# Optimization experiments

Hardware: AMD Instinct MI355X
Metric: run time of the kernel (lower is better)

## Reference

```python
import jax, jax.numpy as jnp
import numpy as np

N = 100000   # nodes
E = 1600000  # edges
FEAT = 128
HID = 128
TGT = 64
L = 3
G = 512      # graphs in batch


def setup_inputs() -> dict:
    key = jax.random.key(0)
    ks = jax.random.split(key, 16)
    s = 0.05
    return {
        "x": jax.random.normal(ks[0], (N, FEAT), jnp.float32),
        "edge_index": jax.random.randint(ks[1], (2, E), 0, N, dtype=jnp.int32),
        "batch": jnp.sort(jax.random.randint(ks[2], (N,), 0, G, dtype=jnp.int32)),
        "conv_w1": jax.random.normal(ks[3], (L, FEAT, HID), jnp.float32) * s,
        "conv_b1": jax.random.normal(ks[4], (L, HID), jnp.float32) * s,
        "conv_w2": jax.random.normal(ks[5], (L, HID, HID), jnp.float32) * s,
        "conv_b2": jax.random.normal(ks[6], (L, HID), jnp.float32) * s,
        "eps": jnp.zeros((L,), jnp.float32),
        "gn_scale": jnp.ones((L, HID), jnp.float32),
        "gn_weight": jnp.ones((L, HID), jnp.float32),
        "gn_bias": jnp.zeros((L, HID), jnp.float32),
        "proj_w1": jax.random.normal(ks[7], (L, HID, HID), jnp.float32) * s,
        "proj_b1": jax.random.normal(ks[8], (L, HID), jnp.float32) * s,
        "proj_w2": jax.random.normal(ks[9], (L, HID, TGT), jnp.float32) * s,
        "proj_b2": jax.random.normal(ks[10], (L, TGT), jnp.float32) * s,
    }


def _graph_norm(h, batch, counts, scale, weight, bias):
    # per-graph mean -> scatter back to nodes
    mean = jax.ops.segment_sum(h, batch, num_segments=G) / counts
    sub = h - mean[batch] * scale
    var = jax.ops.segment_sum(sub * sub, batch, num_segments=G) / counts
    std = jnp.sqrt(var + 1e-8)
    return weight * sub / std[batch] + bias


def reference(x, edge_index, batch, conv_w1, conv_b1, conv_w2, conv_b2, eps,
              gn_scale, gn_weight, gn_bias, proj_w1, proj_b1, proj_w2, proj_b2):
    src, dst = edge_index[0], edge_index[1]
    counts = jnp.maximum(
        jax.ops.segment_sum(jnp.ones((N, 1), x.dtype), batch, num_segments=G), 1.0)
    h = x
    z_cat = []
    for l in range(L):
        # GINConv: aggr_j->i then 2-layer MLP
        aggr = jax.ops.segment_sum(h[src], dst, num_segments=N)
        h = (1.0 + eps[l]) * h + aggr
        h = jax.nn.relu(h @ conv_w1[l] + conv_b1[l]) @ conv_w2[l] + conv_b2[l]
        # GraphNorm
        h = _graph_norm(h, batch, counts, gn_scale[l], gn_weight[l], gn_bias[l])
        h = jax.nn.relu(h)
        # projection MLP + global add pool
        z = jax.nn.relu(h @ proj_w1[l] + proj_b1[l]) @ proj_w2[l] + proj_b2[l]
        z_cat.append(jax.ops.segment_sum(z, batch, num_segments=G))
    return jnp.concatenate(z_cat, axis=-1)  # [G, L*TGT]
```

## Files before the change

### kernel.cpp

```cpp
#include <hip/hip_runtime.h>

#define NN 100000
#define EE 1600000
#define HIDD 128
#define TGTT 64
#define GGG 512
#define NBK 98
#define CAPB 17408
#define ABLK 800
#define EPB 2000
#define CVT2 512
#define LSTR 136
#define GBLK 782
#define OUTB 128

typedef unsigned short ushort_t;
typedef __attribute__((ext_vector_type(8))) short short8;
typedef __attribute__((ext_vector_type(4))) float f32x4;
typedef __attribute__((ext_vector_type(4))) unsigned short us4;

__device__ __forceinline__ float b2f(ushort_t u) {
    union { unsigned int i; float f; } v; v.i = ((unsigned int)u) << 16; return v.f;
}
__device__ __forceinline__ ushort_t f2b(float f) {
    union { float f; unsigned int i; } v; v.f = f;
    unsigned int r = (v.i + 0x7fffu + ((v.i >> 16) & 1u)) >> 16;
    return (ushort_t)r;
}

__global__ __launch_bounds__(256) void k_pro(const float* __restrict__ x, ushort_t* __restrict__ Xb,
                                             const float* __restrict__ cw1, const float* __restrict__ cw2,
                                             const float* __restrict__ pw1, ushort_t* __restrict__ Wt,
                                             const int* __restrict__ batch, int* __restrict__ goff,
                                             const int* __restrict__ ei, int* __restrict__ gcnt,
                                             unsigned int* __restrict__ bbuf) {
    __shared__ int cnt[NBK], base[NBK], cur[NBK];
    int b = blockIdx.x, t = threadIdx.x;

    if (b < ABLK) {
        if (t < NBK) cnt[t] = 0;
        __syncthreads();
        int e0 = b * EPB;
        int e1 = min(e0 + EPB, EE);
        for (int e = e0 + t; e < e1; e += 256)
            atomicAdd(&cnt[ei[EE + e] >> 10], 1);
        __syncthreads();
        if (t < NBK) { base[t] = atomicAdd(&gcnt[t], cnt[t]); cur[t] = 0; }
        __syncthreads();
        for (int e = e0 + t; e < e1; e += 256) {
            int s = ei[e], d = ei[EE + e];
            int bk = d >> 10;
            int off = base[bk] + atomicAdd(&cur[bk], 1);
            if (off < CAPB)
                bbuf[(long)bk * CAPB + off] = (unsigned int)s | (((unsigned int)d & 1023u) << 17);
        }
        return;
    }
    b -= ABLK;
    if (b < CVT2) {
        long total = (long)NN * HIDD / 4;
        long step = (long)CVT2 * 256;
        for (long i = (long)b * 256 + t; i < total; i += step) {
            float4 v = ((const float4*)x)[i];
            us4 o; o.x = f2b(v.x); o.y = f2b(v.y); o.z = f2b(v.z); o.w = f2b(v.w);
            ((us4*)Xb)[i] = o;
        }
        return;
    }
    b -= CVT2;
    if (b < 9) {
        int l = b / 3, j = b % 3;
        const float* src = (j == 0 ? cw1 : j == 1 ? cw2 : pw1) + (size_t)l * HIDD * HIDD;
        ushort_t* dst = Wt + (size_t)b * HIDD * HIDD;
        for (int i = t; i < HIDD * HIDD; i += 256)
            dst[(i & 127) * HIDD + (i >> 7)] = f2b(src[i]);
        return;
    }
    b -= 9;
    {
        int g = b * 256 + t;
        if (g > GGG) return;
        int lo = 0, hi = NN;
        while (lo < hi) { int mid = (lo + hi) >> 1; if (batch[mid] < g) lo = mid + 1; else hi = mid; }
        goff[g] = lo;
    }
}

__global__ __launch_bounds__(1024) void k_csr(const int* __restrict__ gcnt,
                                              const unsigned int* __restrict__ bbuf,
                                              int* __restrict__ rowptr, int* __restrict__ csr) {
    __shared__ int ldeg[1024], tsum[1024], sb[NBK];
    int b = blockIdx.x, t = threadIdx.x;
    if (t < NBK) sb[t] = gcnt[t];
    ldeg[t] = 0;
    __syncthreads();
    if (t == 0) { int a = 0; for (int i = 0; i < NBK; i++) { int v = sb[i]; sb[i] = a; a += v; } }
    __syncthreads();
    int cnt = min(gcnt[b], CAPB);
    int base = sb[b];
    const unsigned int* bb = bbuf + (long)b * CAPB;
    for (int i = t; i < cnt; i += 1024) atomicAdd(&ldeg[bb[i] >> 17], 1);
    __syncthreads();
    int d0 = ldeg[t];
    tsum[t] = d0;
    __syncthreads();
    for (int off = 1; off < 1024; off <<= 1) {
        int u = (t >= off) ? tsum[t - off] : 0;
        __syncthreads();
        tsum[t] += u;
        __syncthreads();
    }
    int p0 = base + tsum[t] - d0;
    int gnode = b * 1024 + t;
    if (gnode < NN) rowptr[gnode] = p0;
    if (b == NBK - 1 && t == 0) rowptr[NN] = EE;
    ldeg[t] = p0;
    __syncthreads();
    for (int i = t; i < cnt; i += 1024) {
        unsigned int en = bb[i];
        int pos = atomicAdd(&ldeg[en >> 17], 1);
        csr[pos] = (int)(en & 0x1FFFFu);
    }
}

__global__ __launch_bounds__(256) void k_gmlp(const ushort_t* __restrict__ hin,
                                              const int* __restrict__ rowptr,
                                              const int* __restrict__ csr,
                                              const float* __restrict__ eps, int l,
                                              const ushort_t* __restrict__ Wt1, const float* __restrict__ B1,
                                              const ushort_t* __restrict__ Wt2, const float* __restrict__ B2,
                                              ushort_t* __restrict__ Y,
                                              const float* __restrict__ pooledP, const int* __restrict__ goff,
                                              const float* __restrict__ WoP, const float* __restrict__ BoP,
                                              float* __restrict__ outP, int lprev) {
    __shared__ ushort_t sX[128 * LSTR];
    int tid = threadIdx.x;

    if (blockIdx.x >= GBLK) {
        if (lprev < 0) return;
        int ob = blockIdx.x - GBLK;
        int sub = tid >> 6, tt = tid & 63;
        int g = ob * 4 + sub;
        if (g >= GGG) return;
        float cntg = (float)(goff[g + 1] - goff[g]);
        float acc = cntg * BoP[tt];
        const float* p = pooledP + (long)g * HIDD;
        for (int k = 0; k < HIDD; k++) acc += p[k] * WoP[k * TGTT + tt];
        outP[(long)g * (3 * TGTT) + lprev * TGTT + tt] = acc;
        return;
    }

    long base = (long)blockIdx.x * 128;
    int lane = tid & 15, ng = tid >> 4;
    int off = lane << 3;
    float e1 = 1.0f + eps[l];

#pragma unroll 1
    for (int it = 0; it < 8; it++) {
        int row = it * 16 + ng;
        long node = base + row;
        short8 o = (short8)0;
        if (node < NN) {
            short8 h = *(const short8*)(hin + (node << 7) + off);
            float acc[8];
#pragma unroll
            for (int t = 0; t < 8; t++) acc[t] = e1 * b2f((ushort_t)h[t]);
            int jb = rowptr[node], je = rowptr[node + 1];
            int j = jb;
            for (; j + 8 <= je; j += 8) {
                int s0 = csr[j], s1 = csr[j + 1], s2 = csr[j + 2], s3 = csr[j + 3];
                int s4 = csr[j + 4], s5 = csr[j + 5], s6 = csr[j + 6], s7 = csr[j + 7];
                short8 v0 = *(const short8*)(hin + ((long)s0 << 7) + off);
                short8 v1 = *(const short8*)(hin + ((long)s1 << 7) + off);
                short8 v2 = *(const short8*)(hin + ((long)s2 << 7) + off);
                short8 v3 = *(const short8*)(hin + ((long)s3 << 7) + off);
                short8 v4 = *(const short8*)(hin + ((long)s4 << 7) + off);
                short8 v5 = *(const short8*)(hin + ((long)s5 << 7) + off);
                short8 v6 = *(const short8*)(hin + ((long)s6 << 7) + off);
                short8 v7 = *(const short8*)(hin + ((long)s7 << 7) + off);
#pragma unroll
                for (int t = 0; t < 8; t++)
                    acc[t] += ((b2f((ushort_t)v0[t]) + b2f((ushort_t)v1[t])) +
                               (b2f((ushort_t)v2[t]) + b2f((ushort_t)v3[t]))) +
                              ((b2f((ushort_t)v4[t]) + b2f((ushort_t)v5[t])) +
                               (b2f((ushort_t)v6[t]) + b2f((ushort_t)v7[t])));
            }
            for (; j + 4 <= je; j += 4) {
                int s0 = csr[j], s1 = csr[j + 1], s2 = csr[j + 2], s3 = csr[j + 3];
                short8 v0 = *(const short8*)(hin + ((long)s0 << 7) + off);
                short8 v1 = *(const short8*)(hin + ((long)s1 << 7) + off);
                short8 v2 = *(const short8*)(hin + ((long)s2 << 7) + off);
                short8 v3 = *(const short8*)(hin + ((long)s3 << 7) + off);
#pragma unroll
                for (int t = 0; t < 8; t++)
                    acc[t] += (b2f((ushort_t)v0[t]) + b2f((ushort_t)v1[t])) +
                              (b2f((ushort_t)v2[t]) + b2f((ushort_t)v3[t]));
            }
            for (; j < je; j++) {
                int s = csr[j];
                short8 v = *(const short8*)(hin + ((long)s << 7) + off);
#pragma unroll
                for (int t = 0; t < 8; t++) acc[t] += b2f((ushort_t)v[t]);
            }
#pragma unroll
            for (int t = 0; t < 8; t++) o[t] = (short)f2b(acc[t]);
        }
        *(short8*)(sX + row * LSTR + off) = o;
    }
    __syncthreads();

    int w = tid >> 6, l64 = tid & 63, q = l64 >> 4, l16 = l64 & 15;
    int r0 = w * 16, r1 = 64 + w * 16;
    short8 a0[4], a1[4];
#pragma unroll
    for (int c = 0; c < 4; c++) {
        a0[c] = *(const short8*)(sX + (r0 + l16) * LSTR + q * 8 + c * 32);
        a1[c] = *(const short8*)(sX + (r1 + l16) * LSTR + q * 8 + c * 32);
    }
    f32x4 acc0[8], acc1[8];
#pragma unroll
    for (int nt = 0; nt < 8; nt++) {
        int col = nt * 16 + l16;
        float bias = B1[col];
        f32x4 c0 = {bias, bias, bias, bias};
        f32x4 c1 = c0;
        const ushort_t* bB = Wt1 + col * HIDD + q * 8;
#pragma unroll
        for (int c = 0; c < 4; c++) {
            short8 b = *(const short8*)(bB + c * 32);
            c0 = __builtin_amdgcn_mfma_f32_16x16x32_bf16(a0[c], b, c0, 0, 0, 0);
            c1 = __builtin_amdgcn_mfma_f32_16x16x32_bf16(a1[c], b, c1, 0, 0, 0);
        }
        acc0[nt] = c0; acc1[nt] = c1;
    }
#pragma unroll
    for (int nt = 0; nt < 8; nt++) {
        int col = nt * 16 + l16;
#pragma unroll
        for (int r = 0; r < 4; r++) {
            sX[(r0 + q * 4 + r) * LSTR + col] = f2b(fmaxf(acc0[nt][r], 0.f));
            sX[(r1 + q * 4 + r) * LSTR + col] = f2b(fmaxf(acc1[nt][r], 0.f));
        }
    }
#pragma unroll
    for (int c = 0; c < 4; c++) {
        a0[c] = *(const short8*)(sX + (r0 + l16) * LSTR + q * 8 + c * 32);
        a1[c] = *(const short8*)(sX + (r1 + l16) * LSTR + q * 8 + c * 32);
    }
#pragma unroll
    for (int nt = 0; nt < 8; nt++) {
        int col = nt * 16 + l16;
        float bias = B2[col];
        f32x4 c0 = {bias, bias, bias, bias};
        f32x4 c1 = c0;
        const ushort_t* bB = Wt2 + col * HIDD + q * 8;
#pragma unroll
        for (int c = 0; c < 4; c++) {
            short8 b = *(const short8*)(bB + c * 32);
            c0 = __builtin_amdgcn_mfma_f32_16x16x32_bf16(a0[c], b, c0, 0, 0, 0);
            c1 = __builtin_amdgcn_mfma_f32_16x16x32_bf16(a1[c], b, c1, 0, 0, 0);
        }
#pragma unroll
        for (int r = 0; r < 4; r++) {
            long row0 = base + r0 + q * 4 + r;
            long row1 = base + r1 + q * 4 + r;
            if (row0 < NN) Y[(row0 << 7) + col] = f2b(c0[r]);
            if (row1 < NN) Y[(row1 << 7) + col] = f2b(c1[r]);
        }
    }
}

__global__ __launch_bounds__(512) void k_gstat(const ushort_t* __restrict__ Hraw,
                                               const int* __restrict__ goff,
                                               const float* __restrict__ scale,
                                               const float* __restrict__ weight,
                                               const float* __restrict__ gnb,
                                               float* __restrict__ Ab, float* __restrict__ Bb,
                                               float* __restrict__ pooled) {
    __shared__ float red[2][32][128];
    int g = blockIdx.x;
    int s = goff[g], e = goff[g + 1];
    float cnt = (float)max(e - s, 1);
    int lane = threadIdx.x & 15;
    int rg = threadIdx.x >> 4;
    int f0 = lane << 3;
    float sum[8], sq[8];
#pragma unroll
    for (int t = 0; t < 8; t++) { sum[t] = 0.f; sq[t] = 0.f; }
    for (int i = s + rg; i < e; i += 32) {
        short8 v = *(const short8*)(Hraw + ((long)i << 7) + f0);
#pragma unroll
        for (int t = 0; t < 8; t++) { float a = b2f((ushort_t)v[t]); sum[t] += a; sq[t] += a * a; }
    }
#pragma unroll
    for (int t = 0; t < 8; t++) { red[0][rg][f0 + t] = sum[t]; red[1][rg][f0 + t] = sq[t]; }
    __syncthreads();
    for (int off = 16; off > 0; off >>= 1) {
        if (rg < off) {
#pragma unroll
            for (int t = 0; t < 8; t++) {
                red[0][rg][f0 + t] += red[0][rg + off][f0 + t];
                red[1][rg][f0 + t] += red[1][rg + off][f0 + t];
            }
        }
        __syncthreads();
    }
    if (rg == 0) {
#pragma unroll
        for (int t = 0; t < 8; t++) {
            int f = f0 + t;
            float mean = red[0][0][f] / cnt;
            float ms = mean * scale[f];
            float var = red[1][0][f] / cnt - 2.f * ms * mean + ms * ms;
            float A = weight[f] / sqrtf(var + 1e-8f);
            Ab[g * HIDD + f] = A;
            Bb[g * HIDD + f] = gnb[f] - ms * A;
            pooled[g * HIDD + f] = 0.f;
        }
    }
}

__global__ __launch_bounds__(256) void k_projpool(const ushort_t* __restrict__ Hraw,
                                                  const int* __restrict__ batch,
                                                  const float* __restrict__ Ab, const float* __restrict__ Bb,
                                                  const ushort_t* __restrict__ Wt, const float* __restrict__ B,
                                                  ushort_t* __restrict__ Hn, float* __restrict__ pooled,
                                                  int store_hn) {
    __shared__ ushort_t sX[128 * LSTR];
    __shared__ int sgid[128];
    __shared__ float sA[4][128], sB[4][128];
    int tid = threadIdx.x;
    long base = (long)blockIdx.x * 128;

    if (tid < 128) sgid[tid] = (base + tid < NN) ? batch[base + tid] : -1;
    __syncthreads();
    int gmin = sgid[0];
    {
        int f = tid & 127;
#pragma unroll
        for (int s = tid >> 7; s < 4; s += 2) {
            int gg = gmin + s;
            if (gg < GGG) {
                sA[s][f] = Ab[(long)gg * HIDD + f];
                sB[s][f] = Bb[(long)gg * HIDD + f];
            }
        }
    }
    __syncthreads();

#pragma unroll
    for (int c = 0; c < 8; c++) {
        int idx = c * 256 + tid;
        int row = idx >> 4, cw = idx & 15;
        long grow = base + row;
        short8 v = (short8)0;
        if (grow < NN) {
            short8 raw = *(const short8*)(Hraw + (grow << 7) + (cw << 3));
            int slot = sgid[row] - gmin;
            const float* pA = &sA[slot][cw << 3];
            const float* pB = &sB[slot][cw << 3];
#pragma unroll
            for (int t = 0; t < 8; t++) {
                float val = b2f((ushort_t)raw[t]) * pA[t] + pB[t];
                v[t] = (short)f2b(val > 0.f ? val : 0.f);
            }
            if (store_hn) *(short8*)(Hn + (grow << 7) + (cw << 3)) = v;
        }
        *(short8*)(sX + row * LSTR + (cw << 3)) = v;
    }
    __syncthreads();

    int w = tid >> 6, l64 = tid & 63, q = l64 >> 4, l16 = l64 & 15;
    int r0 = w * 16, r1 = 64 + w * 16;
    short8 a0[4], a1[4];
#pragma unroll
    for (int c = 0; c < 4; c++) {
        a0[c] = *(const short8*)(sX + (r0 + l16) * LSTR + q * 8 + c * 32);
        a1[c] = *(const short8*)(sX + (r1 + l16) * LSTR + q * 8 + c * 32);
    }
    f32x4 acc0[8], acc1[8];
#pragma unroll
    for (int nt = 0; nt < 8; nt++) {
        int col = nt * 16 + l16;
        float bias = B[col];
        f32x4 c0 = {bias, bias, bias, bias};
        f32x4 c1 = c0;
        const ushort_t* bB = Wt + col * HIDD + q * 8;
#pragma unroll
        for (int c = 0; c < 4; c++) {
            short8 b = *(const short8*)(bB + c * 32);
            c0 = __builtin_amdgcn_mfma_f32_16x16x32_bf16(a0[c], b, c0, 0, 0, 0);
            c1 = __builtin_amdgcn_mfma_f32_16x16x32_bf16(a1[c], b, c1, 0, 0, 0);
        }
        acc0[nt] = c0; acc1[nt] = c1;
    }
#pragma unroll
    for (int nt = 0; nt < 8; nt++) {
        int col = nt * 16 + l16;
#pragma unroll
        for (int r = 0; r < 4; r++) {
            sX[(r0 + q * 4 + r) * LSTR + col] = f2b(fmaxf(acc0[nt][r], 0.f));
            sX[(r1 + q * 4 + r) * LSTR + col] = f2b(fmaxf(acc1[nt][r], 0.f));
        }
    }
    __syncthreads();

    int f = tid & 127, half = tid >> 7;
    int rbeg = half * 64, rend = rbeg + 64;
    float sum = 0.f;
    int curg = -1;
    for (int row = rbeg; row < rend; row++) {
        int g = sgid[row];
        if (g != curg) {
            if (curg >= 0) atomicAdd(&pooled[(long)curg * HIDD + f], sum);
            sum = 0.f; curg = g;
        }
        if (g >= 0) sum += b2f(sX[row * LSTR + f]);
    }
    if (curg >= 0) atomicAdd(&pooled[(long)curg * HIDD + f], sum);
}

__global__ __launch_bounds__(256) void k_out(const float* __restrict__ pooled, const int* __restrict__ goff,
                                             const float* __restrict__ W, const float* __restrict__ B,
                                             float* __restrict__ out, int l) {
    int sub = threadIdx.x >> 6, tt = threadIdx.x & 63;
    int g = blockIdx.x * 4 + sub;
    if (g >= GGG) return;
    float cnt = (float)(goff[g + 1] - goff[g]);
    float acc = cnt * B[tt];
    const float* p = pooled + (long)g * HIDD;
    for (int k = 0; k < HIDD; k++) acc += p[k] * W[k * TGTT + tt];
    out[(long)g * (3 * TGTT) + l * TGTT + tt] = acc;
}

extern "C" void kernel_launch(void* const* d_in, const int* in_sizes, int n_in,
                              void* d_out, int out_size, void* d_ws, size_t ws_size,
                              hipStream_t stream) {
    const float* x    = (const float*)d_in[0];
    const int*   ei   = (const int*)d_in[1];
    const int*   batch= (const int*)d_in[2];
    const float* cw1  = (const float*)d_in[3];
    const float* cb1  = (const float*)d_in[4];
    const float* cw2  = (const float*)d_in[5];
    const float* cb2  = (const float*)d_in[6];
    const float* eps  = (const float*)d_in[7];
    const float* gsc  = (const float*)d_in[8];
    const float* gw   = (const float*)d_in[9];
    const float* gb   = (const float*)d_in[10];
    const float* pw1  = (const float*)d_in[11];
    const float* pb1  = (const float*)d_in[12];
    const float* pw2  = (const float*)d_in[13];
    const float* pb2  = (const float*)d_in[14];
    float* out = (float*)d_out;

    ushort_t* Xb   = (ushort_t*)d_ws;
    ushort_t* Hn   = Xb;
    ushort_t* Hraw = Xb + (size_t)NN * HIDD;
    ushort_t* Wt   = Hraw + (size_t)NN * HIDD;
    float* Ab      = (float*)(Wt + (size_t)9 * HIDD * HIDD);
    float* Bb      = Ab + (size_t)GGG * HIDD;
    float* pooled  = Bb + (size_t)GGG * HIDD;
    int* goff   = (int*)(pooled + (size_t)GGG * HIDD);
    int* rowptr = goff + (GGG + 1);
    int* gcnt   = rowptr + (NN + 1);
    int* csr    = gcnt + NBK;
    unsigned int* bbuf = (unsigned int*)(csr + EE);

    hipMemsetAsync(gcnt, 0, NBK * sizeof(int), stream);
    k_pro<<<ABLK + CVT2 + 9 + 3, 256, 0, stream>>>(x, Xb, cw1, cw2, pw1, Wt, batch, goff, ei, gcnt, bbuf);
    k_csr<<<NBK, 1024, 0, stream>>>(gcnt, bbuf, rowptr, csr);

    for (int l = 0; l < 3; l++) {
        const ushort_t* hin = (l == 0) ? Xb : Hn;
        ushort_t* Wt1 = Wt + (size_t)(l * 3 + 0) * HIDD * HIDD;
        ushort_t* Wt2 = Wt + (size_t)(l * 3 + 1) * HIDD * HIDD;
        ushort_t* Wtp = Wt + (size_t)(l * 3 + 2) * HIDD * HIDD;
        int grid = GBLK + (l > 0 ? OUTB : 0);
        k_gmlp<<<grid, 256, 0, stream>>>(hin, rowptr, csr, eps, l,
                                         Wt1, cb1 + l * HIDD, Wt2, cb2 + l * HIDD, Hraw,
                                         pooled, goff,
                                         pw2 + (size_t)(l - 1) * HIDD * TGTT, pb2 + (l - 1) * TGTT,
                                         out, l - 1);
        k_gstat<<<GGG, 512, 0, stream>>>(Hraw, goff, gsc + l * HIDD, gw + l * HIDD, gb + l * HIDD,
                                         Ab, Bb, pooled);
        k_projpool<<<GBLK, 256, 0, stream>>>(Hraw, batch, Ab, Bb,
                                             Wtp, pb1 + l * HIDD, Hn, pooled, (l < 2) ? 1 : 0);
    }
    k_out<<<OUTB, 256, 0, stream>>>(pooled, goff, pw2 + (size_t)2 * HIDD * TGTT, pb2 + 2 * TGTT, out, 2);
}
```

Measured before the change: 590.3 us.

## Fuse GraphNorm statistics into GIN MLP epilogue with atomic per-graph partial sums

The per-graph sum and sum-of-squares for GraphNorm are now built in the k_gmlp epilogue. Each block stages its bf16 output tile in shared memory, reduces runs of rows that belong to the same graph, and atomically adds the partials into global gsum/gsq buffers. A small k_gfin kernel then turns these into the scale and shift coefficients and zeroes the accumulators for the next layer, so the separate k_gstat pass that re-read all of Hraw is gone. In exchange, float atomics make the sums order-nondeterministic, and the accumulators reuse the bbuf scratch region after CSR construction.

```diff
diff --git a/kernel.cpp b/kernel.cpp
--- a/kernel.cpp
+++ b/kernel.cpp
@@ -126,14 +126,17 @@
 __global__ __launch_bounds__(256) void k_gmlp(const ushort_t* __restrict__ hin,
                                               const int* __restrict__ rowptr,
                                               const int* __restrict__ csr,
+                                              const int* __restrict__ batch,
                                               const float* __restrict__ eps, int l,
                                               const ushort_t* __restrict__ Wt1, const float* __restrict__ B1,
                                               const ushort_t* __restrict__ Wt2, const float* __restrict__ B2,
                                               ushort_t* __restrict__ Y,
+                                              float* __restrict__ gsum, float* __restrict__ gsq,
                                               const float* __restrict__ pooledP, const int* __restrict__ goff,
                                               const float* __restrict__ WoP, const float* __restrict__ BoP,
                                               float* __restrict__ outP, int lprev) {
     __shared__ ushort_t sX[128 * LSTR];
+    __shared__ int sgid[128];
     int tid = threadIdx.x;
 
     if (blockIdx.x >= GBLK) {
@@ -154,6 +157,8 @@
     int lane = tid & 15, ng = tid >> 4;
     int off = lane << 3;
     float e1 = 1.0f + eps[l];
+
+    if (tid < 128) sgid[tid] = (base + tid < NN) ? batch[base + tid] : -1;
 
 #pragma unroll 1
     for (int it = 0; it < 8; it++) {
@@ -264,60 +269,54 @@
         for (int r = 0; r < 4; r++) {
             long row0 = base + r0 + q * 4 + r;
             long row1 = base + r1 + q * 4 + r;
-            if (row0 < NN) Y[(row0 << 7) + col] = f2b(c0[r]);
-            if (row1 < NN) Y[(row1 << 7) + col] = f2b(c1[r]);
-        }
-    }
-}
-
-__global__ __launch_bounds__(512) void k_gstat(const ushort_t* __restrict__ Hraw,
-                                               const int* __restrict__ goff,
-                                               const float* __restrict__ scale,
-                                               const float* __restrict__ weight,
-                                               const float* __restrict__ gnb,
-                                               float* __restrict__ Ab, float* __restrict__ Bb,
-                                               float* __restrict__ pooled) {
-    __shared__ float red[2][32][128];
-    int g = blockIdx.x;
-    int s = goff[g], e = goff[g + 1];
-    float cnt = (float)max(e - s, 1);
-    int lane = threadIdx.x & 15;
-    int rg = threadIdx.x >> 4;
-    int f0 = lane << 3;
-    float sum[8], sq[8];
-#pragma unroll
-    for (int t = 0; t < 8; t++) { sum[t] = 0.f; sq[t] = 0.f; }
-    for (int i = s + rg; i < e; i += 32) {
-        short8 v = *(const short8*)(Hraw + ((long)i << 7) + f0);
-#pragma unroll
-        for (int t = 0; t < 8; t++) { float a = b2f((ushort_t)v[t]); sum[t] += a; sq[t] += a * a; }
-    }
-#pragma unroll
-    for (int t = 0; t < 8; t++) { red[0][rg][f0 + t] = sum[t]; red[1][rg][f0 + t] = sq[t]; }
-    __syncthreads();
-    for (int off = 16; off > 0; off >>= 1) {
-        if (rg < off) {
-#pragma unroll
-            for (int t = 0; t < 8; t++) {
-                red[0][rg][f0 + t] += red[0][rg + off][f0 + t];
-                red[1][rg][f0 + t] += red[1][rg + off][f0 + t];
-            }
-        }
-        __syncthreads();
-    }
-    if (rg == 0) {
-#pragma unroll
-        for (int t = 0; t < 8; t++) {
-            int f = f0 + t;
-            float mean = red[0][0][f] / cnt;
-            float ms = mean * scale[f];
-            float var = red[1][0][f] / cnt - 2.f * ms * mean + ms * ms;
-            float A = weight[f] / sqrtf(var + 1e-8f);
-            Ab[g * HIDD + f] = A;
-            Bb[g * HIDD + f] = gnb[f] - ms * A;
-            pooled[g * HIDD + f] = 0.f;
-        }
-    }
+            ushort_t h0 = f2b(c0[r]), h1 = f2b(c1[r]);
+            if (row0 < NN) Y[(row0 << 7) + col] = h0;
+            if (row1 < NN) Y[(row1 << 7) + col] = h1;
+            sX[(r0 + q * 4 + r) * LSTR + col] = h0;
+            sX[(r1 + q * 4 + r) * LSTR + col] = h1;
+        }
+    }
+    __syncthreads();
+
+    int f = tid & 127, half = tid >> 7;
+    int rbeg = half * 64, rend = rbeg + 64;
+    float s1 = 0.f, s2 = 0.f;
+    int curg = -1;
+    for (int row = rbeg; row < rend; row++) {
+        int g = sgid[row];
+        if (g != curg) {
+            if (curg >= 0) {
+                atomicAdd(&gsum[(long)curg * HIDD + f], s1);
+                atomicAdd(&gsq[(long)curg * HIDD + f], s2);
+            }
+            s1 = 0.f; s2 = 0.f; curg = g;
+        }
+        if (g >= 0) { float a = b2f(sX[row * LSTR + f]); s1 += a; s2 += a * a; }
+    }
+    if (curg >= 0) {
+        atomicAdd(&gsum[(long)curg * HIDD + f], s1);
+        atomicAdd(&gsq[(long)curg * HIDD + f], s2);
+    }
+}
+
+__global__ __launch_bounds__(128) void k_gfin(float* __restrict__ gsum, float* __restrict__ gsq,
+                                              const int* __restrict__ goff,
+                                              const float* __restrict__ scale, const float* __restrict__ weight,
+                                              const float* __restrict__ gnb,
+                                              float* __restrict__ Ab, float* __restrict__ Bb,
+                                              float* __restrict__ pooled) {
+    int g = blockIdx.x, f = threadIdx.x;
+    float cnt = (float)max(goff[g + 1] - goff[g], 1);
+    long i = (long)g * HIDD + f;
+    float mean = gsum[i] / cnt;
+    float ms = mean * scale[f];
+    float var = gsq[i] / cnt - 2.f * ms * mean + ms * ms;
+    float A = weight[f] / sqrtf(var + 1e-8f);
+    Ab[i] = A;
+    Bb[i] = gnb[f] - ms * A;
+    pooled[i] = 0.f;
+    gsum[i] = 0.f;
+    gsq[i] = 0.f;
 }
 
 __global__ __launch_bounds__(256) void k_projpool(const ushort_t* __restrict__ Hraw,
@@ -465,10 +464,13 @@
     int* gcnt   = rowptr + (NN + 1);
     int* csr    = gcnt + NBK;
     unsigned int* bbuf = (unsigned int*)(csr + EE);
+    float* gsum = (float*)bbuf;
+    float* gsq  = gsum + (size_t)GGG * HIDD;
 
     hipMemsetAsync(gcnt, 0, NBK * sizeof(int), stream);
     k_pro<<<ABLK + CVT2 + 9 + 3, 256, 0, stream>>>(x, Xb, cw1, cw2, pw1, Wt, batch, goff, ei, gcnt, bbuf);
     k_csr<<<NBK, 1024, 0, stream>>>(gcnt, bbuf, rowptr, csr);
+    hipMemsetAsync(gsum, 0, (size_t)2 * GGG * HIDD * sizeof(float), stream);
 
     for (int l = 0; l < 3; l++) {
         const ushort_t* hin = (l == 0) ? Xb : Hn;
@@ -476,13 +478,14 @@
         ushort_t* Wt2 = Wt + (size_t)(l * 3 + 1) * HIDD * HIDD;
         ushort_t* Wtp = Wt + (size_t)(l * 3 + 2) * HIDD * HIDD;
         int grid = GBLK + (l > 0 ? OUTB : 0);
-        k_gmlp<<<grid, 256, 0, stream>>>(hin, rowptr, csr, eps, l,
+        k_gmlp<<<grid, 256, 0, stream>>>(hin, rowptr, csr, batch, eps, l,
                                          Wt1, cb1 + l * HIDD, Wt2, cb2 + l * HIDD, Hraw,
+                                         gsum, gsq,
                                          pooled, goff,
                                          pw2 + (size_t)(l - 1) * HIDD * TGTT, pb2 + (l - 1) * TGTT,
                                          out, l - 1);
-        k_gstat<<<GGG, 512, 0, stream>>>(Hraw, goff, gsc + l * HIDD, gw + l * HIDD, gb + l * HIDD,
-                                         Ab, Bb, pooled);
+        k_gfin<<<GGG, 128, 0, stream>>>(gsum, gsq, goff, gsc + l * HIDD, gw + l * HIDD, gb + l * HIDD,
+                                        Ab, Bb, pooled);
         k_projpool<<<GBLK, 256, 0, stream>>>(Hraw, batch, Ab, Bb,
                                              Wtp, pb1 + l * HIDD, Hn, pooled, (l < 2) ? 1 : 0);
     }
```

After: 589.7 us. No clear change (-0.1%).
